# Kernel tuning notes

Hardware: AMD Instinct MI355X
Metric: run time of the kernel (lower is better)

Reference implementation:

```python
import jax, jax.numpy as jnp
import numpy as np

B, N, D, NS, HID, ITERS = 32, 4096, 256, 8, 128, 3
EPS = 1e-8
LN_EPS = 1e-5


def _ln(x, g, b):
    mu = jnp.mean(x, axis=-1, keepdims=True)
    var = jnp.mean(jnp.square(x - mu), axis=-1, keepdims=True)
    return (x - mu) * jax.lax.rsqrt(var + LN_EPS) * g + b


def setup_inputs() -> dict:
    key = jax.random.key(0)
    ks = jax.random.split(key, 32)
    scale = D ** -0.5

    def lin(k, out_d, in_d):
        return jax.random.normal(k, (out_d, in_d), jnp.float32) * (in_d ** -0.5)

    inp = {
        "inputs": jax.random.normal(ks[0], (B, N, D), jnp.float32),
        "slot_noise": jax.random.normal(ks[1], (B, NS, D), jnp.float32),
        "slots_mu": jax.random.uniform(ks[2], (1, 1, D), jnp.float32, -1.0, 1.0) * scale,
        "slots_sigma": jax.random.uniform(ks[3], (1, 1, D), jnp.float32, -1.0, 1.0) * scale,
        "Wq": lin(ks[4], D, D),
        "Wk": lin(ks[5], D, D),
        "Wv": lin(ks[6], D, D),
        "gru_w_ih": lin(ks[7], 3 * D, 2 * D),
        "gru_w_hh": lin(ks[8], 3 * D, D),
        "gru_b_ih": jnp.zeros((3 * D,), jnp.float32),
        "gru_b_hh": jnp.zeros((3 * D,), jnp.float32),
        "obj_w1": lin(ks[9], HID, D),
        "obj_b1": jnp.zeros((HID,), jnp.float32),
        "obj_w2": lin(ks[10], D, HID),
        "obj_b2": jnp.zeros((D,), jnp.float32),
        "rel_w1": lin(ks[11], HID, 2 * D),
        "rel_b1": jnp.zeros((HID,), jnp.float32),
        "rel_w2": lin(ks[12], D, HID),
        "rel_b2": jnp.zeros((D,), jnp.float32),
        "ln_in_g": jnp.ones((D,), jnp.float32),
        "ln_in_b": jnp.zeros((D,), jnp.float32),
        "ln_s_g": jnp.ones((D,), jnp.float32),
        "ln_s_b": jnp.zeros((D,), jnp.float32),
        "ln_ff_g": jnp.ones((D,), jnp.float32),
        "ln_ff_b": jnp.zeros((D,), jnp.float32),
    }
    return inp


def _rel_msg(x, rel_w1, rel_b1, rel_w2, rel_b2):
    # x: (b, n_s, d). rel_mlp(cat(x_i, x_j)) without materializing the concat:
    # split first layer weight into the x_i and x_j halves.
    A = rel_w1[:, :D]   # (hid, d)
    Bm = rel_w1[:, D:]  # (hid, d)
    xa = jnp.einsum('bid,hd->bih', x, A)
    xb = jnp.einsum('bjd,hd->bjh', x, Bm)
    h = jax.nn.relu(xa[:, :, None, :] + xb[:, None, :, :] + rel_b1)  # (b,ns,ns,hid)
    msg = jnp.einsum('bijh,dh->bijd', h, rel_w2) + rel_b2            # (b,ns,ns,d)
    n_s = x.shape[1]
    diag = jnp.eye(n_s, dtype=bool)[None, :, :, None]
    msg = jnp.where(diag, 0.0, msg)
    return msg.sum(axis=2) / (n_s - 1)


def _gru_cell(x, h, w_ih, w_hh, b_ih, b_hh):
    gx = x @ w_ih.T + b_ih  # (B*, 3d)
    gh = h @ w_hh.T + b_hh
    xr, xz, xn = jnp.split(gx, 3, axis=-1)
    hr, hz, hn = jnp.split(gh, 3, axis=-1)
    r = jax.nn.sigmoid(xr + hr)
    z = jax.nn.sigmoid(xz + hz)
    n = jnp.tanh(xn + r * hn)
    return (1.0 - z) * n + z * h


def reference(inputs, slot_noise, slots_mu, slots_sigma, Wq, Wk, Wv,
              gru_w_ih, gru_w_hh, gru_b_ih, gru_b_hh,
              obj_w1, obj_b1, obj_w2, obj_b2,
              rel_w1, rel_b1, rel_w2, rel_b2,
              ln_in_g, ln_in_b, ln_s_g, ln_s_b, ln_ff_g, ln_ff_b):
    b, n, d = inputs.shape
    n_s = slot_noise.shape[1]
    scale = d ** -0.5

    slots = slots_mu + slot_noise * jnp.exp(slots_sigma)  # (b, n_s, d)

    x = _ln(inputs, ln_in_g, ln_in_b)
    k = jnp.einsum('bnd,ed->bne', x, Wk)
    v = jnp.einsum('bnd,ed->bne', x, Wv)

    attns = []
    for _ in range(ITERS):
        slots_prev = slots
        q = jnp.einsum('bid,ed->bie', _ln(slots, ln_s_g, ln_s_b), Wq)
        dots = jnp.einsum('bid,bjd->bij', q, k) * scale        # (b, n_s, n)
        attn = jax.nn.softmax(dots, axis=1) + EPS              # softmax over slots
        attns.append(attn)
        attn_n = attn / attn.sum(axis=-1, keepdims=True)
        updates = jnp.einsum('bjd,bij->bid', v, attn_n)        # (b, n_s, d)
        rel = _rel_msg(slots_prev, rel_w1, rel_b1, rel_w2, rel_b2)
        gin = jnp.concatenate([updates, rel], axis=-1).reshape(b * n_s, 2 * d)
        slots = _gru_cell(gin, slots_prev.reshape(b * n_s, d),
                          gru_w_ih, gru_w_hh, gru_b_ih, gru_b_hh).reshape(b, n_s, d)
        ff = _ln(slots, ln_ff_g, ln_ff_b)
        slots = slots + (jax.nn.relu(ff @ obj_w1.T + obj_b1) @ obj_w2.T + obj_b2)
    return slots, jnp.stack(attns)
```

## Files before the change

kernel.cpp:

```cpp
#include <hip/hip_runtime.h>
#include <hip/hip_bf16.h>
#include <math.h>

static constexpr int Bc   = 32;
static constexpr int Nc   = 4096;
static constexpr int Dc   = 256;
static constexpr int NSc  = 8;
static constexpr int HIDc = 128;
static constexpr int ITERSc = 3;
#define EPSf 1e-8f
#define LN_EPSf 1e-5f

typedef __attribute__((ext_vector_type(8))) short bf16x8;
typedef __attribute__((ext_vector_type(8))) unsigned short u16x8;
typedef __attribute__((ext_vector_type(4))) float f32x4;

__device__ __forceinline__ float bf2f(unsigned int u) {
  return __uint_as_float((u & 0xffffu) << 16);
}

__device__ __forceinline__ unsigned short f2bfu(float f) {
  unsigned int u = __float_as_uint(f);
  unsigned int r = (u + 0x7fffu + ((u >> 16) & 1u)) >> 16;
  return (unsigned short)r;
}

__device__ __forceinline__ void bf8_to_f(uint4 r, float* o) {
  o[0] = bf2f(r.x); o[1] = bf2f(r.x >> 16);
  o[2] = bf2f(r.y); o[3] = bf2f(r.y >> 16);
  o[4] = bf2f(r.z); o[5] = bf2f(r.z >> 16);
  o[6] = bf2f(r.w); o[7] = bf2f(r.w >> 16);
}

__device__ __forceinline__ void gl_lds16(const void* g, void* l) {
  __builtin_amdgcn_global_load_lds(
      (__attribute__((address_space(1))) void*)(g),
      (__attribute__((address_space(3))) void*)(l), 16, 0, 0);
}

__device__ __forceinline__ float block_sum(float v, float* tmp) {
  #pragma unroll
  for (int o = 32; o > 0; o >>= 1) v += __shfl_down(v, o, 64);
  int lane = threadIdx.x & 63, wid = threadIdx.x >> 6;
  __syncthreads();
  if (lane == 0) tmp[wid] = v;
  __syncthreads();
  return tmp[0] + tmp[1] + tmp[2] + tmp[3];
}

__device__ __forceinline__ float sigmf(float x) { return 1.f / (1.f + expf(-x)); }

__global__ __launch_bounds__(256) void k_init_slots(const float* __restrict__ noise,
                                                    const float* __restrict__ mu,
                                                    const float* __restrict__ sigma,
                                                    float* __restrict__ slots) {
  int idx = blockIdx.x * 256 + threadIdx.x;
  int d = idx & (Dc - 1);
  slots[idx] = mu[d] + noise[idx] * expf(sigma[d]);
}

__global__ __launch_bounds__(256) void k_stats(const float* __restrict__ inp,
                                               float2* __restrict__ stats) {
  __shared__ float tmp[4];
  int t = threadIdx.x;
  size_t row0 = (size_t)blockIdx.x * 8;
  for (int r = 0; r < 8; r++) {
    float x = inp[(row0 + r) * Dc + t];
    float s = block_sum(x, tmp);
    float m = s * (1.0f / Dc);
    float dx = x - m;
    float s2 = block_sum(dx * dx, tmp);
    float rs = rsqrtf(s2 * (1.0f / Dc) + LN_EPSf);
    if (t == 0) stats[row0 + r] = make_float2(m, rs);
  }
}

__global__ __launch_bounds__(256) void k_wcvt(const float* __restrict__ Wk,
                                              const float* __restrict__ Wv,
                                              unsigned short* __restrict__ wbuf) {
  int idx = blockIdx.x * 256 + threadIdx.x;
  int n = idx >> 8, k = idx & 255;
  float v = (n < 256) ? Wk[n * 256 + k] : Wv[(n - 256) * 256 + k];
  wbuf[idx] = f2bfu(v);
}

__global__ __launch_bounds__(256) void k_wprep(const float* __restrict__ w_ih,
                                               const float* __restrict__ w_hh,
                                               unsigned short* __restrict__ Wcat) {
  int idx = blockIdx.x * 256 + threadIdx.x;
  int o = idx / 768, c = idx - o * 768;
  float v = (c < 512) ? w_ih[o * 512 + c] : w_hh[o * 256 + (c - 512)];
  Wcat[idx] = f2bfu(v);
}

#define BM 128
#define BN 128
#define BK 64
__global__ __launch_bounds__(256) void k_gemm_kv(const float* __restrict__ inp,
                                                 const float2* __restrict__ stats,
                                                 const float* __restrict__ lng,
                                                 const float* __restrict__ lnb,
                                                 const unsigned short* __restrict__ wbuf,
                                                 unsigned short* __restrict__ kbuf,
                                                 unsigned short* __restrict__ vbuf) {
  __shared__ unsigned short Als[BM * BK];
  __shared__ unsigned short Bls[BN * BK];
  int tid = threadIdx.x;
  int lane = tid & 63, w = tid >> 6;
  int idx16 = lane & 15, quad = lane >> 4;
  int m0 = (blockIdx.x >> 2) * BM;
  int n0 = (blockIdx.x & 3) * BN;
  int wm = w & 1, wn = w >> 1;

  f32x4 acc[4][4];
  #pragma unroll
  for (int i = 0; i < 4; i++)
    #pragma unroll
    for (int j = 0; j < 4; j++) acc[i][j] = (f32x4){0.f, 0.f, 0.f, 0.f};

  for (int kt = 0; kt < 4; kt++) {
    int k0 = kt * BK;
    #pragma unroll
    for (int c = 0; c < 4; c++) {
      int idx = (w * 4 + c) * 64 + lane;
      int row = idx >> 3, lc = idx & 7;
      int gc = lc ^ (row & 7);
      const char* gsrc = (const char*)wbuf + ((size_t)(n0 + row) * 256 + k0) * 2 + gc * 16;
      char* ldst = (char*)Bls + (size_t)(w * 4 + c) * 1024;
      gl_lds16(gsrc, ldst);
    }
    #pragma unroll
    for (int p = 0; p < 4; p++) {
      int idx = p * 256 + tid;
      int row = idx >> 3, c8 = idx & 7;
      const float* src = inp + (size_t)(m0 + row) * 256 + k0 + c8 * 8;
      float2 st = stats[m0 + row];
      float4 x0 = *(const float4*)(src);
      float4 x1 = *(const float4*)(src + 4);
      float4 g0 = *(const float4*)(lng + k0 + c8 * 8);
      float4 g1 = *(const float4*)(lng + k0 + c8 * 8 + 4);
      float4 b0 = *(const float4*)(lnb + k0 + c8 * 8);
      float4 b1 = *(const float4*)(lnb + k0 + c8 * 8 + 4);
      u16x8 pk;
      pk[0] = f2bfu((x0.x - st.x) * st.y * g0.x + b0.x);
      pk[1] = f2bfu((x0.y - st.x) * st.y * g0.y + b0.y);
      pk[2] = f2bfu((x0.z - st.x) * st.y * g0.z + b0.z);
      pk[3] = f2bfu((x0.w - st.x) * st.y * g0.w + b0.w);
      pk[4] = f2bfu((x1.x - st.x) * st.y * g1.x + b1.x);
      pk[5] = f2bfu((x1.y - st.x) * st.y * g1.y + b1.y);
      pk[6] = f2bfu((x1.z - st.x) * st.y * g1.z + b1.z);
      pk[7] = f2bfu((x1.w - st.x) * st.y * g1.w + b1.w);
      int dchunk = c8 ^ (row & 7);
      *(u16x8*)((char*)Als + (size_t)(row * 8 + dchunk) * 16) = pk;
    }
    __syncthreads();
    #pragma unroll
    for (int ks = 0; ks < 2; ks++) {
      bf16x8 af[4], bfr[4];
      int kchunk = ks * 4 + quad;
      #pragma unroll
      for (int mt = 0; mt < 4; mt++) {
        int row = wm * 64 + mt * 16 + idx16;
        af[mt] = *(const bf16x8*)((const char*)Als + (size_t)(row * 8 + (kchunk ^ (row & 7))) * 16);
      }
      #pragma unroll
      for (int nt = 0; nt < 4; nt++) {
        int row = wn * 64 + nt * 16 + idx16;
        bfr[nt] = *(const bf16x8*)((const char*)Bls + (size_t)(row * 8 + (kchunk ^ (row & 7))) * 16);
      }
      #pragma unroll
      for (int mt = 0; mt < 4; mt++)
        #pragma unroll
        for (int nt = 0; nt < 4; nt++)
          acc[mt][nt] = __builtin_amdgcn_mfma_f32_16x16x32_bf16(af[mt], bfr[nt], acc[mt][nt], 0, 0, 0);
    }
    __syncthreads();
  }
  unsigned short* dst = (n0 < 256) ? kbuf : vbuf;
  int coff = (n0 < 256) ? n0 : (n0 - 256);
  #pragma unroll
  for (int mt = 0; mt < 4; mt++) {
    #pragma unroll
    for (int nt = 0; nt < 4; nt++) {
      int gm = m0 + wm * 64 + mt * 16 + quad * 4;
      int col = coff + wn * 64 + nt * 16 + idx16;
      #pragma unroll
      for (int r = 0; r < 4; r++)
        dst[(size_t)(gm + r) * 256 + col] = f2bfu(acc[mt][nt][r]);
    }
  }
}

__global__ __launch_bounds__(256) void k_qproj0(const float* __restrict__ slots,
                                                const float* __restrict__ Wq,
                                                const float* __restrict__ g,
                                                const float* __restrict__ bb_,
                                                float* __restrict__ q,
                                                float* __restrict__ S,
                                                float* __restrict__ updraw) {
  __shared__ float xs[Dc];
  __shared__ float tmp[4];
  int t = threadIdx.x;
  int row = blockIdx.x;
  updraw[row * 256 + t] = 0.f;
  if (blockIdx.x == 0) S[t] = 0.f;
  float x = slots[row * Dc + t];
  float s = block_sum(x, tmp);
  float m = s * (1.0f / Dc);
  float dx = x - m;
  float s2 = block_sum(dx * dx, tmp);
  float rs = rsqrtf(s2 * (1.0f / Dc) + LN_EPSf);
  xs[t] = dx * rs * g[t] + bb_[t];
  __syncthreads();
  float acc = 0.f;
  const float4* wq4 = (const float4*)(Wq + t * Dc);
  for (int d4 = 0; d4 < Dc / 4; d4++) {
    float4 w = wq4[d4];
    float4 x4 = *(const float4*)&xs[d4 * 4];
    acc += w.x * x4.x + w.y * x4.y + w.z * x4.z + w.w * x4.w;
  }
  q[row * Dc + t] = acc;
}

__global__ __launch_bounds__(256) void k_attn(const float* __restrict__ q,
                                              const unsigned short* __restrict__ kbuf,
                                              const unsigned short* __restrict__ vbuf,
                                              float* __restrict__ attn,
                                              float* __restrict__ S,
                                              float* __restrict__ updraw) {
  __shared__ float qs[NSc][Dc];
  __shared__ float at[NSc][512];
  __shared__ float parts[2][NSc][256];
  __shared__ float tmp[4];
  int t = threadIdx.x;
  int b = blockIdx.x >> 3;
  int jc = blockIdx.x & 7;
  for (int x = t; x < NSc * Dc; x += 256) qs[x >> 8][x & 255] = q[b * NSc * Dc + x];
  __syncthreads();
  int jA = jc * 512 + t;
  const unsigned short* k0 = kbuf + ((size_t)b * Nc + jA) * Dc;
  const unsigned short* k1 = k0 + (size_t)256 * Dc;
  float dot[2][NSc];
  #pragma unroll
  for (int jj = 0; jj < 2; jj++)
    #pragma unroll
    for (int i = 0; i < NSc; i++) dot[jj][i] = 0.f;
  for (int d8 = 0; d8 < Dc / 8; d8++) {
    float kv0[8], kv1[8];
    bf8_to_f(*(const uint4*)(k0 + d8 * 8), kv0);
    bf8_to_f(*(const uint4*)(k1 + d8 * 8), kv1);
    #pragma unroll
    for (int i = 0; i < NSc; i++) {
      const float* qr = &qs[i][d8 * 8];
      float s0 = 0.f, s1 = 0.f;
      #pragma unroll
      for (int u = 0; u < 8; u++) { s0 += kv0[u] * qr[u]; s1 += kv1[u] * qr[u]; }
      dot[0][i] += s0; dot[1][i] += s1;
    }
  }
  float a[2][NSc];
  #pragma unroll
  for (int jj = 0; jj < 2; jj++) {
    float m = -1e30f;
    #pragma unroll
    for (int i = 0; i < NSc; i++) { float s = dot[jj][i] * 0.0625f; dot[jj][i] = s; m = fmaxf(m, s); }
    float sum = 0.f;
    #pragma unroll
    for (int i = 0; i < NSc; i++) { float e = expf(dot[jj][i] - m); a[jj][i] = e; sum += e; }
    float inv = 1.f / sum;
    #pragma unroll
    for (int i = 0; i < NSc; i++) a[jj][i] = a[jj][i] * inv + EPSf;
  }
  float* ab = attn + (size_t)b * NSc * Nc;
  #pragma unroll
  for (int i = 0; i < NSc; i++) {
    ab[i * Nc + jA] = a[0][i];
    ab[i * Nc + jA + 256] = a[1][i];
    at[i][t] = a[0][i];
    at[i][t + 256] = a[1][i];
  }
  for (int i = 0; i < NSc; i++) {
    float bs = block_sum(a[0][i] + a[1][i], tmp);
    if (t == 0) atomicAdd(&S[b * NSc + i], bs);
  }
  __syncthreads();
  int rs = t >> 7, dg = t & 127;
  float acc[NSc][2];
  #pragma unroll
  for (int i = 0; i < NSc; i++) { acc[i][0] = 0.f; acc[i][1] = 0.f; }
  const unsigned short* vr = vbuf + ((size_t)b * Nc + jc * 512 + rs * 256) * Dc + dg * 2;
  for (int j = 0; j < 256; j++) {
    unsigned int vv = *(const unsigned int*)(vr + (size_t)j * Dc);
    float v0 = bf2f(vv), v1 = bf2f(vv >> 16);
    #pragma unroll
    for (int i = 0; i < NSc; i++) {
      float a_ = at[i][rs * 256 + j];
      acc[i][0] += a_ * v0;
      acc[i][1] += a_ * v1;
    }
  }
  #pragma unroll
  for (int i = 0; i < NSc; i++) {
    parts[rs][i][dg * 2] = acc[i][0];
    parts[rs][i][dg * 2 + 1] = acc[i][1];
  }
  __syncthreads();
  for (int i = 0; i < NSc; i++) {
    float val = parts[0][i][t] + parts[1][i][t];
    atomicAdd(&updraw[(b * NSc + i) * 256 + t], val);
  }
}

__global__ __launch_bounds__(256) void k_slot_a(const float* __restrict__ slots,
                                                const float* __restrict__ updraw,
                                                const float* __restrict__ S,
                                                const float* __restrict__ w1,
                                                const float* __restrict__ b1,
                                                const float* __restrict__ w2,
                                                const float* __restrict__ b2,
                                                unsigned short* __restrict__ Xb) {
  __shared__ float sp[NSc][256];
  __shared__ float xa[4][128];
  __shared__ float xb[NSc][128];
  __shared__ float hs[4][128];
  int t = threadIdx.x;
  int b = blockIdx.x >> 1, half = blockIdx.x & 1;
  int i0 = half * 4;
  for (int x = t; x < NSc * 256; x += 256) sp[x >> 8][x & 255] = slots[b * NSc * 256 + x];
  __syncthreads();
  for (int r = 0; r < 4; r++) {
    int grow = b * NSc + i0 + r;
    float u = updraw[grow * 256 + t] / S[grow];
    Xb[(size_t)grow * 768 + t] = f2bfu(u);
    Xb[(size_t)grow * 768 + 512 + t] = f2bfu(sp[i0 + r][t]);
  }
  int h = t & 127;
  {
    int jg = t >> 7;
    const float* wr = w1 + h * 512 + 256;
    float acc[4] = {0.f, 0.f, 0.f, 0.f};
    for (int d = 0; d < 256; d += 4) {
      float4 wv = *(const float4*)(wr + d);
      #pragma unroll
      for (int j = 0; j < 4; j++) {
        const float* s4 = &sp[jg * 4 + j][d];
        acc[j] += wv.x * s4[0] + wv.y * s4[1] + wv.z * s4[2] + wv.w * s4[3];
      }
    }
    #pragma unroll
    for (int j = 0; j < 4; j++) xb[jg * 4 + j][h] = acc[j];
  }
  {
    int rg = t >> 7;
    const float* wr = w1 + h * 512;
    float acc[2] = {0.f, 0.f};
    for (int d = 0; d < 256; d += 4) {
      float4 wv = *(const float4*)(wr + d);
      #pragma unroll
      for (int rr = 0; rr < 2; rr++) {
        const float* s4 = &sp[i0 + rg * 2 + rr][d];
        acc[rr] += wv.x * s4[0] + wv.y * s4[1] + wv.z * s4[2] + wv.w * s4[3];
      }
    }
    #pragma unroll
    for (int rr = 0; rr < 2; rr++) xa[rg * 2 + rr][h] = acc[rr];
  }
  __syncthreads();
  {
    float bv = b1[h];
    int ig = t >> 7;
    #pragma unroll
    for (int ii = 0; ii < 2; ii++) {
      int il = ig * 2 + ii;
      int ibatch = i0 + il;
      float av = xa[il][h];
      float s = 0.f;
      #pragma unroll
      for (int j = 0; j < NSc; j++) {
        if (j == ibatch) continue;
        s += fmaxf(av + xb[j][h] + bv, 0.f);
      }
      hs[il][h] = s;
    }
  }
  __syncthreads();
  {
    const float* w2r = w2 + t * 128;
    float acc[4] = {0.f, 0.f, 0.f, 0.f};
    for (int hh = 0; hh < 128; hh += 4) {
      float4 wv = *(const float4*)(w2r + hh);
      #pragma unroll
      for (int r = 0; r < 4; r++) {
        const float* h4 = &hs[r][hh];
        acc[r] += wv.x * h4[0] + wv.y * h4[1] + wv.z * h4[2] + wv.w * h4[3];
      }
    }
    float bv2 = b2[t];
    for (int r = 0; r < 4; r++) {
      float rel = acc[r] * (1.0f / 7.0f) + bv2;
      Xb[(size_t)(b * NSc + i0 + r) * 768 + 256 + t] = f2bfu(rel);
    }
  }
}

__global__ __launch_bounds__(256) void k_gates(const unsigned short* __restrict__ Xb,
                                               const unsigned short* __restrict__ Wcat,
                                               unsigned short* __restrict__ Yb) {
  __shared__ unsigned short Als[64 * 64];
  __shared__ unsigned short Bls[64 * 64];
  int tid = threadIdx.x;
  int lane = tid & 63, w = tid >> 6;
  int idx16 = lane & 15, quad = lane >> 4;
  int m0 = (blockIdx.x / 12) * 64;
  int n0 = (blockIdx.x % 12) * 64;
  int wm = w & 1, wn = w >> 1;
  f32x4 acc[2][2];
  #pragma unroll
  for (int i = 0; i < 2; i++)
    #pragma unroll
    for (int j = 0; j < 2; j++) acc[i][j] = (f32x4){0.f, 0.f, 0.f, 0.f};

  for (int kt = 0; kt < 12; kt++) {
    int k0 = kt * 64;
    #pragma unroll
    for (int c = 0; c < 2; c++) {
      int idx = (w * 2 + c) * 64 + lane;
      int row = idx >> 3, lc = idx & 7;
      int gc = lc ^ (row & 7);
      gl_lds16((const char*)Xb + (size_t)(m0 + row) * 1536 + k0 * 2 + gc * 16,
               (char*)Als + (size_t)(w * 2 + c) * 1024);
      gl_lds16((const char*)Wcat + (size_t)(n0 + row) * 1536 + k0 * 2 + gc * 16,
               (char*)Bls + (size_t)(w * 2 + c) * 1024);
    }
    __syncthreads();
    #pragma unroll
    for (int ks = 0; ks < 2; ks++) {
      bf16x8 af[2], bfr[2];
      int kchunk = ks * 4 + quad;
      #pragma unroll
      for (int mt = 0; mt < 2; mt++) {
        int row = wm * 32 + mt * 16 + idx16;
        af[mt] = *(const bf16x8*)((const char*)Als + (size_t)(row * 8 + (kchunk ^ (row & 7))) * 16);
      }
      #pragma unroll
      for (int nt = 0; nt < 2; nt++) {
        int row = wn * 32 + nt * 16 + idx16;
        bfr[nt] = *(const bf16x8*)((const char*)Bls + (size_t)(row * 8 + (kchunk ^ (row & 7))) * 16);
      }
      #pragma unroll
      for (int mt = 0; mt < 2; mt++)
        #pragma unroll
        for (int nt = 0; nt < 2; nt++)
          acc[mt][nt] = __builtin_amdgcn_mfma_f32_16x16x32_bf16(af[mt], bfr[nt], acc[mt][nt], 0, 0, 0);
    }
    __syncthreads();
  }
  #pragma unroll
  for (int mt = 0; mt < 2; mt++) {
    #pragma unroll
    for (int nt = 0; nt < 2; nt++) {
      int gm = m0 + wm * 32 + mt * 16 + quad * 4;
      int col = n0 + wn * 32 + nt * 16 + idx16;
      #pragma unroll
      for (int r = 0; r < 4; r++)
        Yb[(size_t)(gm + r) * 768 + col] = f2bfu(acc[mt][nt][r]);
    }
  }
}

__global__ __launch_bounds__(256) void k_slot_c(const unsigned short* __restrict__ Yb,
                                                const float* __restrict__ w_hh,
                                                const float* __restrict__ b_ih,
                                                const float* __restrict__ b_hh,
                                                float* __restrict__ slots,
                                                const float* __restrict__ ow1,
                                                const float* __restrict__ ob1,
                                                const float* __restrict__ ow2,
                                                const float* __restrict__ ob2,
                                                const float* __restrict__ lng,
                                                const float* __restrict__ lnb,
                                                const float* __restrict__ lsg,
                                                const float* __restrict__ lsb,
                                                const float* __restrict__ Wq,
                                                float* __restrict__ qbuf,
                                                float* __restrict__ updraw,
                                                float* __restrict__ S,
                                                float* __restrict__ outf,
                                                int wfinal) {
  __shared__ float sp4[4][256];
  __shared__ float ffl[4][256];
  __shared__ float h1l[4][128];
  __shared__ float xs2[4][256];
  __shared__ float tmp[4];
  int t = threadIdx.x;
  int g0 = blockIdx.x * 4;
  for (int x = t; x < 1024; x += 256) sp4[x >> 8][x & 255] = slots[(size_t)g0 * 256 + x];
  __syncthreads();
  float hn_raw[4] = {0.f, 0.f, 0.f, 0.f};
  {
    const float* whr = w_hh + (size_t)(512 + t) * 256;
    for (int d = 0; d < 256; d += 4) {
      float4 wv = *(const float4*)(whr + d);
      #pragma unroll
      for (int r = 0; r < 4; r++) {
        const float* s4 = &sp4[r][d];
        hn_raw[r] += wv.x * s4[0] + wv.y * s4[1] + wv.z * s4[2] + wv.w * s4[3];
      }
    }
  }
  float bir = b_ih[t], bhr = b_hh[t];
  float biz = b_ih[256 + t], bhz = b_hh[256 + t];
  float bin_ = b_ih[512 + t], bhn = b_hh[512 + t];
  float snew[4];
  #pragma unroll
  for (int r = 0; r < 4; r++) {
    size_t yoff = (size_t)(g0 + r) * 768;
    float yr = bf2f((unsigned int)Yb[yoff + t]);
    float yz = bf2f((unsigned int)Yb[yoff + 256 + t]);
    float yx = bf2f((unsigned int)Yb[yoff + 512 + t]);
    float rg = sigmf(yr + bir + bhr);
    float zg = sigmf(yz + biz + bhz);
    float hn = hn_raw[r] + bhn;
    float xn = (yx - hn_raw[r]) + bin_;
    float ng = tanhf(xn + rg * hn);
    snew[r] = (1.f - zg) * ng + zg * sp4[r][t];
  }
  for (int r = 0; r < 4; r++) {
    float s = block_sum(snew[r], tmp);
    float m = s * (1.0f / 256.0f);
    float dx = snew[r] - m;
    float s2 = block_sum(dx * dx, tmp);
    float rs = rsqrtf(s2 * (1.0f / 256.0f) + LN_EPSf);
    ffl[r][t] = dx * rs * lng[t] + lnb[t];
  }
  __syncthreads();
  {
    int h = t & 127, rg2 = t >> 7;
    const float* w1r = ow1 + h * 256;
    float acc[2] = {0.f, 0.f};
    for (int d = 0; d < 256; d += 4) {
      float4 wv = *(const float4*)(w1r + d);
      #pragma unroll
      for (int rr = 0; rr < 2; rr++) {
        const float* f4 = &ffl[rg2 * 2 + rr][d];
        acc[rr] += wv.x * f4[0] + wv.y * f4[1] + wv.z * f4[2] + wv.w * f4[3];
      }
    }
    float bo = ob1[h];
    #pragma unroll
    for (int rr = 0; rr < 2; rr++) h1l[rg2 * 2 + rr][h] = fmaxf(acc[rr] + bo, 0.f);
  }
  __syncthreads();
  float res[4];
  {
    const float* w2r = ow2 + t * 128;
    float acc[4] = {0.f, 0.f, 0.f, 0.f};
    for (int hh = 0; hh < 128; hh += 4) {
      float4 wv = *(const float4*)(w2r + hh);
      #pragma unroll
      for (int r = 0; r < 4; r++) {
        const float* h4 = &h1l[r][hh];
        acc[r] += wv.x * h4[0] + wv.y * h4[1] + wv.z * h4[2] + wv.w * h4[3];
      }
    }
    float bo2 = ob2[t];
    #pragma unroll
    for (int r = 0; r < 4; r++) res[r] = snew[r] + acc[r] + bo2;
  }
  #pragma unroll
  for (int r = 0; r < 4; r++) {
    slots[(size_t)(g0 + r) * 256 + t] = res[r];
    if (wfinal) outf[(size_t)(g0 + r) * 256 + t] = res[r];
  }
  for (int r = 0; r < 4; r++) {
    float s = block_sum(res[r], tmp);
    float m = s * (1.0f / 256.0f);
    float dx = res[r] - m;
    float s2 = block_sum(dx * dx, tmp);
    float rs = rsqrtf(s2 * (1.0f / 256.0f) + LN_EPSf);
    xs2[r][t] = dx * rs * lsg[t] + lsb[t];
  }
  __syncthreads();
  {
    const float* wqr = Wq + t * 256;
    float acc[4] = {0.f, 0.f, 0.f, 0.f};
    for (int d = 0; d < 256; d += 4) {
      float4 wv = *(const float4*)(wqr + d);
      #pragma unroll
      for (int r = 0; r < 4; r++) {
        const float* x4 = &xs2[r][d];
        acc[r] += wv.x * x4[0] + wv.y * x4[1] + wv.z * x4[2] + wv.w * x4[3];
      }
    }
    #pragma unroll
    for (int r = 0; r < 4; r++) qbuf[(size_t)(g0 + r) * 256 + t] = acc[r];
  }
  #pragma unroll
  for (int r = 0; r < 4; r++) updraw[(size_t)(g0 + r) * 256 + t] = 0.f;
  if (t < 4) S[g0 + t] = 0.f;
}

extern "C" void kernel_launch(void* const* d_in, const int* in_sizes, int n_in,
                              void* d_out, int out_size, void* d_ws, size_t ws_size,
                              hipStream_t stream) {
  const float* inputs      = (const float*)d_in[0];
  const float* slot_noise  = (const float*)d_in[1];
  const float* slots_mu    = (const float*)d_in[2];
  const float* slots_sigma = (const float*)d_in[3];
  const float* Wq          = (const float*)d_in[4];
  const float* Wk          = (const float*)d_in[5];
  const float* Wv          = (const float*)d_in[6];
  const float* gru_w_ih    = (const float*)d_in[7];
  const float* gru_w_hh    = (const float*)d_in[8];
  const float* gru_b_ih    = (const float*)d_in[9];
  const float* gru_b_hh    = (const float*)d_in[10];
  const float* obj_w1      = (const float*)d_in[11];
  const float* obj_b1      = (const float*)d_in[12];
  const float* obj_w2      = (const float*)d_in[13];
  const float* obj_b2      = (const float*)d_in[14];
  const float* rel_w1      = (const float*)d_in[15];
  const float* rel_b1      = (const float*)d_in[16];
  const float* rel_w2      = (const float*)d_in[17];
  const float* rel_b2      = (const float*)d_in[18];
  const float* ln_in_g     = (const float*)d_in[19];
  const float* ln_in_b     = (const float*)d_in[20];
  const float* ln_s_g      = (const float*)d_in[21];
  const float* ln_s_b      = (const float*)d_in[22];
  const float* ln_ff_g     = (const float*)d_in[23];
  const float* ln_ff_b     = (const float*)d_in[24];

  char* w = (char*)d_ws;
  unsigned short* kbuf = (unsigned short*)(w);
  unsigned short* vbuf = (unsigned short*)(w + (size_t)67108864);
  float* qbuf   = (float*)(w + (size_t)134217728);
  float* slots  = (float*)(w + (size_t)134479872);
  float* updraw = (float*)(w + (size_t)134742016);
  float* Sbuf   = (float*)(w + (size_t)135004160);
  unsigned short* Wcat = (unsigned short*)(w + (size_t)135008256);
  float2* stats = (float2*)(w + (size_t)135008256);
  unsigned short* Xbuf = (unsigned short*)(w + (size_t)136187904);
  unsigned short* wbuf = (unsigned short*)(w + (size_t)136187904);
  unsigned short* Ybuf = (unsigned short*)(w + (size_t)136581120);

  float* out = (float*)d_out;
  float* attn_base = out + (size_t)Bc * NSc * Dc;

  k_init_slots<<<Bc * NSc * Dc / 256, 256, 0, stream>>>(slot_noise, slots_mu, slots_sigma, slots);
  k_wcvt<<<512, 256, 0, stream>>>(Wk, Wv, wbuf);
  k_stats<<<Bc * Nc / 8, 256, 0, stream>>>(inputs, stats);
  k_gemm_kv<<<(Bc * Nc / BM) * 4, 256, 0, stream>>>(inputs, stats, ln_in_g, ln_in_b,
                                                    wbuf, kbuf, vbuf);
  k_wprep<<<768 * 768 / 256, 256, 0, stream>>>(gru_w_ih, gru_w_hh, Wcat);
  k_qproj0<<<Bc * NSc, 256, 0, stream>>>(slots, Wq, ln_s_g, ln_s_b, qbuf, Sbuf, updraw);

  for (int it = 0; it < ITERSc; it++) {
    float* attn = attn_base + (size_t)it * Bc * NSc * Nc;
    k_attn<<<Bc * 8, 256, 0, stream>>>(qbuf, kbuf, vbuf, attn, Sbuf, updraw);
    k_slot_a<<<Bc * 2, 256, 0, stream>>>(slots, updraw, Sbuf,
                                         rel_w1, rel_b1, rel_w2, rel_b2, Xbuf);
    k_gates<<<4 * 12, 256, 0, stream>>>(Xbuf, Wcat, Ybuf);
    k_slot_c<<<64, 256, 0, stream>>>(Ybuf, gru_w_hh, gru_b_ih, gru_b_hh, slots,
                                     obj_w1, obj_b1, obj_w2, obj_b2,
                                     ln_ff_g, ln_ff_b, ln_s_g, ln_s_b, Wq,
                                     qbuf, updraw, Sbuf,
                                     out, it == ITERSc - 1 ? 1 : 0);
  }
}
```

Baseline: 771.4 us.

## Fuse input LayerNorm stats into KV GEMM, pre-transpose small weights to bf16, retile attention

The separate LayerNorm statistics pass is removed: the KV GEMM now computes per-row mean and rstd itself with wave shuffles and uses 64-row tiles covering all 512 K/V output columns, so the input is read once per tile. Small weights (rel, obj, Wq, the W_hh n-gate block) are pre-transposed and converted to bf16 in a new prep kernel, giving coalesced reads in the slot kernels. The attention kernel now runs twice as many blocks, each handling 256 tokens, and q is stored as bf16. LayerNorms in the slot kernels switch to single-pass shuffle reductions, which trades some numerical accuracy (one-pass variance, bf16 weights and q) for less memory traffic and fewer barriers.

```diff
diff --git a/kernel.cpp b/kernel.cpp
--- a/kernel.cpp
+++ b/kernel.cpp
@@ -15,6 +15,15 @@
 typedef __attribute__((ext_vector_type(8))) unsigned short u16x8;
 typedef __attribute__((ext_vector_type(4))) float f32x4;
 
+static constexpr int W1AT = 0;
+static constexpr int W1BT = 32768;
+static constexpr int W2T  = 65536;
+static constexpr int OW1T = 98304;
+static constexpr int OW2T = 131072;
+static constexpr int WQT  = 163840;
+static constexpr int WHNT = 229376;
+static constexpr int TW_ELEMS = 294912;
+
 __device__ __forceinline__ float bf2f(unsigned int u) {
   return __uint_as_float((u & 0xffffu) << 16);
 }
@@ -59,22 +68,6 @@
   slots[idx] = mu[d] + noise[idx] * expf(sigma[d]);
 }
 
-__global__ __launch_bounds__(256) void k_stats(const float* __restrict__ inp,
-                                               float2* __restrict__ stats) {
-  __shared__ float tmp[4];
-  int t = threadIdx.x;
-  size_t row0 = (size_t)blockIdx.x * 8;
-  for (int r = 0; r < 8; r++) {
-    float x = inp[(row0 + r) * Dc + t];
-    float s = block_sum(x, tmp);
-    float m = s * (1.0f / Dc);
-    float dx = x - m;
-    float s2 = block_sum(dx * dx, tmp);
-    float rs = rsqrtf(s2 * (1.0f / Dc) + LN_EPSf);
-    if (t == 0) stats[row0 + r] = make_float2(m, rs);
-  }
-}
-
 __global__ __launch_bounds__(256) void k_wcvt(const float* __restrict__ Wk,
                                               const float* __restrict__ Wv,
                                               unsigned short* __restrict__ wbuf) {
@@ -89,52 +82,85 @@
                                                unsigned short* __restrict__ Wcat) {
   int idx = blockIdx.x * 256 + threadIdx.x;
   int o = idx / 768, c = idx - o * 768;
-  float v = (c < 512) ? w_ih[o * 512 + c] : w_hh[o * 256 + (c - 512)];
+  float v;
+  if (c < 512) v = w_ih[o * 512 + c];
+  else v = (o < 512) ? w_hh[o * 256 + (c - 512)] : 0.f;
   Wcat[idx] = f2bfu(v);
 }
 
-#define BM 128
-#define BN 128
-#define BK 64
-__global__ __launch_bounds__(256) void k_gemm_kv(const float* __restrict__ inp,
-                                                 const float2* __restrict__ stats,
-                                                 const float* __restrict__ lng,
-                                                 const float* __restrict__ lnb,
-                                                 const unsigned short* __restrict__ wbuf,
-                                                 unsigned short* __restrict__ kbuf,
-                                                 unsigned short* __restrict__ vbuf) {
-  __shared__ unsigned short Als[BM * BK];
-  __shared__ unsigned short Bls[BN * BK];
+__global__ __launch_bounds__(256) void k_tprep(const float* __restrict__ rel_w1,
+                                               const float* __restrict__ rel_w2,
+                                               const float* __restrict__ obj_w1,
+                                               const float* __restrict__ obj_w2,
+                                               const float* __restrict__ Wq,
+                                               const float* __restrict__ w_hh,
+                                               unsigned short* __restrict__ Tw) {
+  int i = blockIdx.x * 256 + threadIdx.x;
+  if (i >= TW_ELEMS) return;
+  float v;
+  if (i < W1BT) { int j = i - W1AT; int d = j >> 7, h = j & 127; v = rel_w1[h * 512 + d]; }
+  else if (i < W2T)  { int j = i - W1BT; int d = j >> 7, h = j & 127; v = rel_w1[h * 512 + 256 + d]; }
+  else if (i < OW1T) { int j = i - W2T;  int h = j >> 8, o = j & 255; v = rel_w2[o * 128 + h]; }
+  else if (i < OW2T) { int j = i - OW1T; int d = j >> 7, h = j & 127; v = obj_w1[h * 256 + d]; }
+  else if (i < WQT)  { int j = i - OW2T; int h = j >> 8, o = j & 255; v = obj_w2[o * 128 + h]; }
+  else if (i < WHNT) { int j = i - WQT;  int d = j >> 8, e = j & 255; v = Wq[e * 256 + d]; }
+  else               { int j = i - WHNT; int d = j >> 8, o = j & 255; v = w_hh[(512 + o) * 256 + d]; }
+  Tw[i] = f2bfu(v);
+}
+
+__global__ __launch_bounds__(256, 2) void k_gemm_kv(const float* __restrict__ inp,
+                                                    const float* __restrict__ lng,
+                                                    const float* __restrict__ lnb,
+                                                    const unsigned short* __restrict__ wbuf,
+                                                    unsigned short* __restrict__ kbuf,
+                                                    unsigned short* __restrict__ vbuf) {
+  __shared__ unsigned short Als[64 * 64];
+  __shared__ unsigned short Bls[512 * 64];
+  __shared__ float smu[64];
+  __shared__ float srs[64];
   int tid = threadIdx.x;
   int lane = tid & 63, w = tid >> 6;
   int idx16 = lane & 15, quad = lane >> 4;
-  int m0 = (blockIdx.x >> 2) * BM;
-  int n0 = (blockIdx.x & 3) * BN;
-  int wm = w & 1, wn = w >> 1;
-
-  f32x4 acc[4][4];
+  int m0 = blockIdx.x * 64;
+
+  for (int rr = 0; rr < 16; rr++) {
+    int row = w * 16 + rr;
+    float4 v = *(const float4*)(inp + (size_t)(m0 + row) * 256 + lane * 4);
+    float s = v.x + v.y + v.z + v.w;
+    float q = v.x * v.x + v.y * v.y + v.z * v.z + v.w * v.w;
+    #pragma unroll
+    for (int o = 32; o > 0; o >>= 1) { s += __shfl_down(s, o, 64); q += __shfl_down(q, o, 64); }
+    if (lane == 0) {
+      float mu = s * (1.0f / 256.0f);
+      float var = q * (1.0f / 256.0f) - mu * mu;
+      smu[row] = mu;
+      srs[row] = rsqrtf(var + LN_EPSf);
+    }
+  }
+  __syncthreads();
+
+  f32x4 acc[4][8];
   #pragma unroll
   for (int i = 0; i < 4; i++)
     #pragma unroll
-    for (int j = 0; j < 4; j++) acc[i][j] = (f32x4){0.f, 0.f, 0.f, 0.f};
+    for (int j = 0; j < 8; j++) acc[i][j] = (f32x4){0.f, 0.f, 0.f, 0.f};
 
   for (int kt = 0; kt < 4; kt++) {
-    int k0 = kt * BK;
-    #pragma unroll
-    for (int c = 0; c < 4; c++) {
-      int idx = (w * 4 + c) * 64 + lane;
+    int k0 = kt * 64;
+    #pragma unroll
+    for (int c = 0; c < 16; c++) {
+      int idx = (w * 16 + c) * 64 + lane;
       int row = idx >> 3, lc = idx & 7;
       int gc = lc ^ (row & 7);
-      const char* gsrc = (const char*)wbuf + ((size_t)(n0 + row) * 256 + k0) * 2 + gc * 16;
-      char* ldst = (char*)Bls + (size_t)(w * 4 + c) * 1024;
-      gl_lds16(gsrc, ldst);
-    }
-    #pragma unroll
-    for (int p = 0; p < 4; p++) {
+      gl_lds16((const char*)wbuf + ((size_t)row * 256 + k0) * 2 + gc * 16,
+               (char*)Bls + (size_t)(w * 16 + c) * 1024);
+    }
+    #pragma unroll
+    for (int p = 0; p < 2; p++) {
       int idx = p * 256 + tid;
       int row = idx >> 3, c8 = idx & 7;
       const float* src = inp + (size_t)(m0 + row) * 256 + k0 + c8 * 8;
-      float2 st = stats[m0 + row];
+      float mu = smu[row], rs = srs[row];
       float4 x0 = *(const float4*)(src);
       float4 x1 = *(const float4*)(src + 4);
       float4 g0 = *(const float4*)(lng + k0 + c8 * 8);
@@ -142,60 +168,60 @@
       float4 b0 = *(const float4*)(lnb + k0 + c8 * 8);
       float4 b1 = *(const float4*)(lnb + k0 + c8 * 8 + 4);
       u16x8 pk;
-      pk[0] = f2bfu((x0.x - st.x) * st.y * g0.x + b0.x);
-      pk[1] = f2bfu((x0.y - st.x) * st.y * g0.y + b0.y);
-      pk[2] = f2bfu((x0.z - st.x) * st.y * g0.z + b0.z);
-      pk[3] = f2bfu((x0.w - st.x) * st.y * g0.w + b0.w);
-      pk[4] = f2bfu((x1.x - st.x) * st.y * g1.x + b1.x);
-      pk[5] = f2bfu((x1.y - st.x) * st.y * g1.y + b1.y);
-      pk[6] = f2bfu((x1.z - st.x) * st.y * g1.z + b1.z);
-      pk[7] = f2bfu((x1.w - st.x) * st.y * g1.w + b1.w);
+      pk[0] = f2bfu((x0.x - mu) * rs * g0.x + b0.x);
+      pk[1] = f2bfu((x0.y - mu) * rs * g0.y + b0.y);
+      pk[2] = f2bfu((x0.z - mu) * rs * g0.z + b0.z);
+      pk[3] = f2bfu((x0.w - mu) * rs * g0.w + b0.w);
+      pk[4] = f2bfu((x1.x - mu) * rs * g1.x + b1.x);
+      pk[5] = f2bfu((x1.y - mu) * rs * g1.y + b1.y);
+      pk[6] = f2bfu((x1.z - mu) * rs * g1.z + b1.z);
+      pk[7] = f2bfu((x1.w - mu) * rs * g1.w + b1.w);
       int dchunk = c8 ^ (row & 7);
       *(u16x8*)((char*)Als + (size_t)(row * 8 + dchunk) * 16) = pk;
     }
     __syncthreads();
     #pragma unroll
     for (int ks = 0; ks < 2; ks++) {
-      bf16x8 af[4], bfr[4];
       int kchunk = ks * 4 + quad;
+      bf16x8 af[4], bfr[8];
       #pragma unroll
       for (int mt = 0; mt < 4; mt++) {
-        int row = wm * 64 + mt * 16 + idx16;
+        int row = mt * 16 + idx16;
         af[mt] = *(const bf16x8*)((const char*)Als + (size_t)(row * 8 + (kchunk ^ (row & 7))) * 16);
       }
       #pragma unroll
-      for (int nt = 0; nt < 4; nt++) {
-        int row = wn * 64 + nt * 16 + idx16;
+      for (int nt = 0; nt < 8; nt++) {
+        int row = w * 128 + nt * 16 + idx16;
         bfr[nt] = *(const bf16x8*)((const char*)Bls + (size_t)(row * 8 + (kchunk ^ (row & 7))) * 16);
       }
       #pragma unroll
       for (int mt = 0; mt < 4; mt++)
         #pragma unroll
-        for (int nt = 0; nt < 4; nt++)
+        for (int nt = 0; nt < 8; nt++)
           acc[mt][nt] = __builtin_amdgcn_mfma_f32_16x16x32_bf16(af[mt], bfr[nt], acc[mt][nt], 0, 0, 0);
     }
     __syncthreads();
   }
-  unsigned short* dst = (n0 < 256) ? kbuf : vbuf;
-  int coff = (n0 < 256) ? n0 : (n0 - 256);
   #pragma unroll
   for (int mt = 0; mt < 4; mt++) {
     #pragma unroll
-    for (int nt = 0; nt < 4; nt++) {
-      int gm = m0 + wm * 64 + mt * 16 + quad * 4;
-      int col = coff + wn * 64 + nt * 16 + idx16;
+    for (int nt = 0; nt < 8; nt++) {
+      int gm = m0 + mt * 16 + quad * 4;
+      int col = w * 128 + nt * 16 + idx16;
+      unsigned short* dst = (col < 256) ? kbuf : vbuf;
+      int c = col & 255;
       #pragma unroll
       for (int r = 0; r < 4; r++)
-        dst[(size_t)(gm + r) * 256 + col] = f2bfu(acc[mt][nt][r]);
+        dst[(size_t)(gm + r) * 256 + c] = f2bfu(acc[mt][nt][r]);
     }
   }
 }
 
 __global__ __launch_bounds__(256) void k_qproj0(const float* __restrict__ slots,
-                                                const float* __restrict__ Wq,
+                                                const unsigned short* __restrict__ Tw,
                                                 const float* __restrict__ g,
                                                 const float* __restrict__ bb_,
-                                                float* __restrict__ q,
+                                                unsigned short* __restrict__ qb,
                                                 float* __restrict__ S,
                                                 float* __restrict__ updraw) {
   __shared__ float xs[Dc];
@@ -213,96 +239,93 @@
   xs[t] = dx * rs * g[t] + bb_[t];
   __syncthreads();
   float acc = 0.f;
-  const float4* wq4 = (const float4*)(Wq + t * Dc);
-  for (int d4 = 0; d4 < Dc / 4; d4++) {
-    float4 w = wq4[d4];
-    float4 x4 = *(const float4*)&xs[d4 * 4];
-    acc += w.x * x4.x + w.y * x4.y + w.z * x4.z + w.w * x4.w;
-  }
-  q[row * Dc + t] = acc;
-}
-
-__global__ __launch_bounds__(256) void k_attn(const float* __restrict__ q,
+  const unsigned short* wq = Tw + WQT;
+  for (int d = 0; d < 256; d++) acc += bf2f(wq[d * 256 + t]) * xs[d];
+  qb[row * 256 + t] = f2bfu(acc);
+}
+
+__global__ __launch_bounds__(256) void k_attn(const unsigned short* __restrict__ qb,
                                               const unsigned short* __restrict__ kbuf,
                                               const unsigned short* __restrict__ vbuf,
                                               float* __restrict__ attn,
                                               float* __restrict__ S,
                                               float* __restrict__ updraw) {
   __shared__ float qs[NSc][Dc];
-  __shared__ float at[NSc][512];
+  __shared__ float at[NSc][256];
   __shared__ float parts[2][NSc][256];
-  __shared__ float tmp[4];
   int t = threadIdx.x;
-  int b = blockIdx.x >> 3;
-  int jc = blockIdx.x & 7;
-  for (int x = t; x < NSc * Dc; x += 256) qs[x >> 8][x & 255] = q[b * NSc * Dc + x];
-  __syncthreads();
-  int jA = jc * 512 + t;
-  const unsigned short* k0 = kbuf + ((size_t)b * Nc + jA) * Dc;
-  const unsigned short* k1 = k0 + (size_t)256 * Dc;
-  float dot[2][NSc];
-  #pragma unroll
-  for (int jj = 0; jj < 2; jj++)
-    #pragma unroll
-    for (int i = 0; i < NSc; i++) dot[jj][i] = 0.f;
+  int b = blockIdx.x >> 4;
+  int jc = blockIdx.x & 15;
+  int j0 = jc * 256;
+  for (int x = t; x < NSc * Dc; x += 256) qs[x >> 8][x & 255] = bf2f(qb[b * NSc * Dc + x]);
+  __syncthreads();
+  int j = j0 + t;
+  const uint4* krow = (const uint4*)(kbuf + ((size_t)b * Nc + j) * Dc);
+  float dot[NSc];
+  #pragma unroll
+  for (int i = 0; i < NSc; i++) dot[i] = 0.f;
   for (int d8 = 0; d8 < Dc / 8; d8++) {
-    float kv0[8], kv1[8];
-    bf8_to_f(*(const uint4*)(k0 + d8 * 8), kv0);
-    bf8_to_f(*(const uint4*)(k1 + d8 * 8), kv1);
+    float kv[8];
+    bf8_to_f(krow[d8], kv);
     #pragma unroll
     for (int i = 0; i < NSc; i++) {
       const float* qr = &qs[i][d8 * 8];
-      float s0 = 0.f, s1 = 0.f;
-      #pragma unroll
-      for (int u = 0; u < 8; u++) { s0 += kv0[u] * qr[u]; s1 += kv1[u] * qr[u]; }
-      dot[0][i] += s0; dot[1][i] += s1;
-    }
-  }
-  float a[2][NSc];
-  #pragma unroll
-  for (int jj = 0; jj < 2; jj++) {
-    float m = -1e30f;
-    #pragma unroll
-    for (int i = 0; i < NSc; i++) { float s = dot[jj][i] * 0.0625f; dot[jj][i] = s; m = fmaxf(m, s); }
-    float sum = 0.f;
-    #pragma unroll
-    for (int i = 0; i < NSc; i++) { float e = expf(dot[jj][i] - m); a[jj][i] = e; sum += e; }
-    float inv = 1.f / sum;
-    #pragma unroll
-    for (int i = 0; i < NSc; i++) a[jj][i] = a[jj][i] * inv + EPSf;
-  }
+      float s0 = 0.f;
+      #pragma unroll
+      for (int u = 0; u < 8; u++) s0 += kv[u] * qr[u];
+      dot[i] += s0;
+    }
+  }
+  float m = -1e30f;
+  #pragma unroll
+  for (int i = 0; i < NSc; i++) { float s = dot[i] * 0.0625f; dot[i] = s; m = fmaxf(m, s); }
+  float sum = 0.f;
+  float a[NSc];
+  #pragma unroll
+  for (int i = 0; i < NSc; i++) { float e = expf(dot[i] - m); a[i] = e; sum += e; }
+  float inv = 1.f / sum;
+  #pragma unroll
+  for (int i = 0; i < NSc; i++) a[i] = a[i] * inv + EPSf;
   float* ab = attn + (size_t)b * NSc * Nc;
   #pragma unroll
   for (int i = 0; i < NSc; i++) {
-    ab[i * Nc + jA] = a[0][i];
-    ab[i * Nc + jA + 256] = a[1][i];
-    at[i][t] = a[0][i];
-    at[i][t + 256] = a[1][i];
-  }
+    ab[i * Nc + j] = a[i];
+    at[i][t] = a[i];
+  }
+  __syncthreads();
+  {
+    int wv = t >> 6, lane = t & 63;
+    #pragma unroll
+    for (int ii = 0; ii < 2; ii++) {
+      int i = wv + ii * 4;
+      float4 v = *(const float4*)&at[i][lane * 4];
+      float s = v.x + v.y + v.z + v.w;
+      #pragma unroll
+      for (int o = 32; o > 0; o >>= 1) s += __shfl_down(s, o, 64);
+      if (lane == 0) atomicAdd(&S[b * NSc + i], s);
+    }
+  }
+  int rsh = t >> 7, dg = t & 127;
+  float acc[NSc][2];
+  #pragma unroll
+  for (int i = 0; i < NSc; i++) { acc[i][0] = 0.f; acc[i][1] = 0.f; }
+  const unsigned short* vr = vbuf + ((size_t)b * Nc + j0 + rsh * 128) * Dc + dg * 2;
+  for (int jj = 0; jj < 128; jj += 2) {
+    unsigned int v0 = *(const unsigned int*)(vr + (size_t)jj * Dc);
+    unsigned int v1 = *(const unsigned int*)(vr + (size_t)(jj + 1) * Dc);
+    float v0a = bf2f(v0), v0b = bf2f(v0 >> 16);
+    float v1a = bf2f(v1), v1b = bf2f(v1 >> 16);
+    #pragma unroll
+    for (int i = 0; i < NSc; i++) {
+      float2 ap = *(const float2*)&at[i][rsh * 128 + jj];
+      acc[i][0] += ap.x * v0a + ap.y * v1a;
+      acc[i][1] += ap.x * v0b + ap.y * v1b;
+    }
+  }
+  #pragma unroll
   for (int i = 0; i < NSc; i++) {
-    float bs = block_sum(a[0][i] + a[1][i], tmp);
-    if (t == 0) atomicAdd(&S[b * NSc + i], bs);
-  }
-  __syncthreads();
-  int rs = t >> 7, dg = t & 127;
-  float acc[NSc][2];
-  #pragma unroll
-  for (int i = 0; i < NSc; i++) { acc[i][0] = 0.f; acc[i][1] = 0.f; }
-  const unsigned short* vr = vbuf + ((size_t)b * Nc + jc * 512 + rs * 256) * Dc + dg * 2;
-  for (int j = 0; j < 256; j++) {
-    unsigned int vv = *(const unsigned int*)(vr + (size_t)j * Dc);
-    float v0 = bf2f(vv), v1 = bf2f(vv >> 16);
-    #pragma unroll
-    for (int i = 0; i < NSc; i++) {
-      float a_ = at[i][rs * 256 + j];
-      acc[i][0] += a_ * v0;
-      acc[i][1] += a_ * v1;
-    }
-  }
-  #pragma unroll
-  for (int i = 0; i < NSc; i++) {
-    parts[rs][i][dg * 2] = acc[i][0];
-    parts[rs][i][dg * 2 + 1] = acc[i][1];
+    parts[rsh][i][dg * 2] = acc[i][0];
+    parts[rsh][i][dg * 2 + 1] = acc[i][1];
   }
   __syncthreads();
   for (int i = 0; i < NSc; i++) {
@@ -314,14 +337,13 @@
 __global__ __launch_bounds__(256) void k_slot_a(const float* __restrict__ slots,
                                                 const float* __restrict__ updraw,
                                                 const float* __restrict__ S,
-                                                const float* __restrict__ w1,
+                                                const unsigned short* __restrict__ Tw,
                                                 const float* __restrict__ b1,
-                                                const float* __restrict__ w2,
                                                 const float* __restrict__ b2,
                                                 unsigned short* __restrict__ Xb) {
   __shared__ float sp[NSc][256];
-  __shared__ float xa[4][128];
-  __shared__ float xb[NSc][128];
+  __shared__ float xpart[2][12][128];
+  __shared__ float xabl[12][128];
   __shared__ float hs[4][128];
   int t = threadIdx.x;
   int b = blockIdx.x >> 1, half = blockIdx.x & 1;
@@ -334,36 +356,31 @@
     Xb[(size_t)grow * 768 + t] = f2bfu(u);
     Xb[(size_t)grow * 768 + 512 + t] = f2bfu(sp[i0 + r][t]);
   }
-  int h = t & 127;
-  {
-    int jg = t >> 7;
-    const float* wr = w1 + h * 512 + 256;
-    float acc[4] = {0.f, 0.f, 0.f, 0.f};
-    for (int d = 0; d < 256; d += 4) {
-      float4 wv = *(const float4*)(wr + d);
-      #pragma unroll
-      for (int j = 0; j < 4; j++) {
-        const float* s4 = &sp[jg * 4 + j][d];
-        acc[j] += wv.x * s4[0] + wv.y * s4[1] + wv.z * s4[2] + wv.w * s4[3];
-      }
-    }
-    #pragma unroll
-    for (int j = 0; j < 4; j++) xb[jg * 4 + j][h] = acc[j];
-  }
-  {
-    int rg = t >> 7;
-    const float* wr = w1 + h * 512;
-    float acc[2] = {0.f, 0.f};
-    for (int d = 0; d < 256; d += 4) {
-      float4 wv = *(const float4*)(wr + d);
-      #pragma unroll
-      for (int rr = 0; rr < 2; rr++) {
-        const float* s4 = &sp[i0 + rg * 2 + rr][d];
-        acc[rr] += wv.x * s4[0] + wv.y * s4[1] + wv.z * s4[2] + wv.w * s4[3];
-      }
-    }
-    #pragma unroll
-    for (int rr = 0; rr < 2; rr++) xa[rg * 2 + rr][h] = acc[rr];
+  int h = t & 127, dh = t >> 7;
+  {
+    const unsigned short* wa = Tw + W1AT;
+    const unsigned short* wb = Tw + W1BT;
+    float accb[8] = {0, 0, 0, 0, 0, 0, 0, 0};
+    float acca[4] = {0, 0, 0, 0};
+    for (int dd = 0; dd < 128; dd++) {
+      int d = dh * 128 + dd;
+      float wbv = bf2f(wb[d * 128 + h]);
+      float wav = bf2f(wa[d * 128 + h]);
+      #pragma unroll
+      for (int jj = 0; jj < 8; jj++) accb[jj] += wbv * sp[jj][d];
+      #pragma unroll
+      for (int r = 0; r < 4; r++) acca[r] += wav * sp[i0 + r][d];
+    }
+    #pragma unroll
+    for (int jj = 0; jj < 8; jj++) xpart[dh][jj][h] = accb[jj];
+    #pragma unroll
+    for (int r = 0; r < 4; r++) xpart[dh][8 + r][h] = acca[r];
+  }
+  __syncthreads();
+  {
+    int g = t >> 7;
+    for (int jj = g * 6; jj < g * 6 + 6; jj++)
+      xabl[jj][h] = xpart[0][jj][h] + xpart[1][jj][h];
   }
   __syncthreads();
   {
@@ -373,31 +390,28 @@
     for (int ii = 0; ii < 2; ii++) {
       int il = ig * 2 + ii;
       int ibatch = i0 + il;
-      float av = xa[il][h];
+      float av = xabl[8 + il][h];
       float s = 0.f;
       #pragma unroll
-      for (int j = 0; j < NSc; j++) {
-        if (j == ibatch) continue;
-        s += fmaxf(av + xb[j][h] + bv, 0.f);
+      for (int jj = 0; jj < NSc; jj++) {
+        if (jj == ibatch) continue;
+        s += fmaxf(av + xabl[jj][h] + bv, 0.f);
       }
       hs[il][h] = s;
     }
   }
   __syncthreads();
   {
-    const float* w2r = w2 + t * 128;
-    float acc[4] = {0.f, 0.f, 0.f, 0.f};
-    for (int hh = 0; hh < 128; hh += 4) {
-      float4 wv = *(const float4*)(w2r + hh);
-      #pragma unroll
-      for (int r = 0; r < 4; r++) {
-        const float* h4 = &hs[r][hh];
-        acc[r] += wv.x * h4[0] + wv.y * h4[1] + wv.z * h4[2] + wv.w * h4[3];
-      }
+    const unsigned short* w2 = Tw + W2T;
+    float am[4] = {0, 0, 0, 0};
+    for (int hh = 0; hh < 128; hh++) {
+      float wv = bf2f(w2[hh * 256 + t]);
+      #pragma unroll
+      for (int r = 0; r < 4; r++) am[r] += wv * hs[r][hh];
     }
     float bv2 = b2[t];
     for (int r = 0; r < 4; r++) {
-      float rel = acc[r] * (1.0f / 7.0f) + bv2;
+      float rel = am[r] * (1.0f / 7.0f) + bv2;
       Xb[(size_t)(b * NSc + i0 + r) * 768 + 256 + t] = f2bfu(rel);
     }
   }
@@ -469,43 +483,37 @@
 }
 
 __global__ __launch_bounds__(256) void k_slot_c(const unsigned short* __restrict__ Yb,
-                                                const float* __restrict__ w_hh,
+                                                const unsigned short* __restrict__ Tw,
                                                 const float* __restrict__ b_ih,
                                                 const float* __restrict__ b_hh,
                                                 float* __restrict__ slots,
-                                                const float* __restrict__ ow1,
                                                 const float* __restrict__ ob1,
-                                                const float* __restrict__ ow2,
                                                 const float* __restrict__ ob2,
                                                 const float* __restrict__ lng,
                                                 const float* __restrict__ lnb,
                                                 const float* __restrict__ lsg,
                                                 const float* __restrict__ lsb,
-                                                const float* __restrict__ Wq,
-                                                float* __restrict__ qbuf,
+                                                unsigned short* __restrict__ qb,
                                                 float* __restrict__ updraw,
                                                 float* __restrict__ S,
                                                 float* __restrict__ outf,
                                                 int wfinal) {
   __shared__ float sp4[4][256];
   __shared__ float ffl[4][256];
+  __shared__ float h1p[2][4][128];
   __shared__ float h1l[4][128];
   __shared__ float xs2[4][256];
-  __shared__ float tmp[4];
   int t = threadIdx.x;
   int g0 = blockIdx.x * 4;
   for (int x = t; x < 1024; x += 256) sp4[x >> 8][x & 255] = slots[(size_t)g0 * 256 + x];
   __syncthreads();
-  float hn_raw[4] = {0.f, 0.f, 0.f, 0.f};
-  {
-    const float* whr = w_hh + (size_t)(512 + t) * 256;
-    for (int d = 0; d < 256; d += 4) {
-      float4 wv = *(const float4*)(whr + d);
-      #pragma unroll
-      for (int r = 0; r < 4; r++) {
-        const float* s4 = &sp4[r][d];
-        hn_raw[r] += wv.x * s4[0] + wv.y * s4[1] + wv.z * s4[2] + wv.w * s4[3];
-      }
+  float hn[4] = {0, 0, 0, 0};
+  {
+    const unsigned short* wh = Tw + WHNT;
+    for (int d = 0; d < 256; d++) {
+      float wv = bf2f(wh[d * 256 + t]);
+      #pragma unroll
+      for (int r = 0; r < 4; r++) hn[r] += wv * sp4[r][d];
     }
   }
   float bir = b_ih[t], bhr = b_hh[t];
@@ -520,80 +528,105 @@
     float yx = bf2f((unsigned int)Yb[yoff + 512 + t]);
     float rg = sigmf(yr + bir + bhr);
     float zg = sigmf(yz + biz + bhz);
-    float hn = hn_raw[r] + bhn;
-    float xn = (yx - hn_raw[r]) + bin_;
-    float ng = tanhf(xn + rg * hn);
+    float ng = tanhf(yx + bin_ + rg * (hn[r] + bhn));
     snew[r] = (1.f - zg) * ng + zg * sp4[r][t];
-  }
-  for (int r = 0; r < 4; r++) {
-    float s = block_sum(snew[r], tmp);
-    float m = s * (1.0f / 256.0f);
-    float dx = snew[r] - m;
-    float s2 = block_sum(dx * dx, tmp);
-    float rs = rsqrtf(s2 * (1.0f / 256.0f) + LN_EPSf);
-    ffl[r][t] = dx * rs * lng[t] + lnb[t];
-  }
-  __syncthreads();
-  {
-    int h = t & 127, rg2 = t >> 7;
-    const float* w1r = ow1 + h * 256;
-    float acc[2] = {0.f, 0.f};
-    for (int d = 0; d < 256; d += 4) {
-      float4 wv = *(const float4*)(w1r + d);
-      #pragma unroll
-      for (int rr = 0; rr < 2; rr++) {
-        const float* f4 = &ffl[rg2 * 2 + rr][d];
-        acc[rr] += wv.x * f4[0] + wv.y * f4[1] + wv.z * f4[2] + wv.w * f4[3];
-      }
-    }
+    ffl[r][t] = snew[r];
+  }
+  __syncthreads();
+  {
+    int wv = t >> 6, lane = t & 63;
+    float4 v = *(const float4*)&ffl[wv][lane * 4];
+    float s = v.x + v.y + v.z + v.w;
+    float q = v.x * v.x + v.y * v.y + v.z * v.z + v.w * v.w;
+    #pragma unroll
+    for (int o = 32; o > 0; o >>= 1) { s += __shfl_down(s, o, 64); q += __shfl_down(q, o, 64); }
+    s = __shfl(s, 0, 64); q = __shfl(q, 0, 64);
+    float mu = s * (1.0f / 256.0f);
+    float rs = rsqrtf(q * (1.0f / 256.0f) - mu * mu + LN_EPSf);
+    float4 g4 = *(const float4*)&lng[lane * 4];
+    float4 b4 = *(const float4*)&lnb[lane * 4];
+    float4 o4;
+    o4.x = (v.x - mu) * rs * g4.x + b4.x;
+    o4.y = (v.y - mu) * rs * g4.y + b4.y;
+    o4.z = (v.z - mu) * rs * g4.z + b4.z;
+    o4.w = (v.w - mu) * rs * g4.w + b4.w;
+    *(float4*)&ffl[wv][lane * 4] = o4;
+  }
+  __syncthreads();
+  {
+    const unsigned short* w1 = Tw + OW1T;
+    int h = t & 127, dh = t >> 7;
+    float a1[4] = {0, 0, 0, 0};
+    for (int dd = 0; dd < 128; dd++) {
+      int d = dh * 128 + dd;
+      float wv = bf2f(w1[d * 128 + h]);
+      #pragma unroll
+      for (int r = 0; r < 4; r++) a1[r] += wv * ffl[r][d];
+    }
+    #pragma unroll
+    for (int r = 0; r < 4; r++) h1p[dh][r][h] = a1[r];
+  }
+  __syncthreads();
+  {
+    int h = t & 127, g = t >> 7;
     float bo = ob1[h];
     #pragma unroll
-    for (int rr = 0; rr < 2; rr++) h1l[rg2 * 2 + rr][h] = fmaxf(acc[rr] + bo, 0.f);
+    for (int rr = 0; rr < 2; rr++) {
+      int r = g * 2 + rr;
+      h1l[r][h] = fmaxf(h1p[0][r][h] + h1p[1][r][h] + bo, 0.f);
+    }
   }
   __syncthreads();
   float res[4];
   {
-    const float* w2r = ow2 + t * 128;
-    float acc[4] = {0.f, 0.f, 0.f, 0.f};
-    for (int hh = 0; hh < 128; hh += 4) {
-      float4 wv = *(const float4*)(w2r + hh);
-      #pragma unroll
-      for (int r = 0; r < 4; r++) {
-        const float* h4 = &h1l[r][hh];
-        acc[r] += wv.x * h4[0] + wv.y * h4[1] + wv.z * h4[2] + wv.w * h4[3];
-      }
+    const unsigned short* w2 = Tw + OW2T;
+    float ao[4] = {0, 0, 0, 0};
+    for (int hh = 0; hh < 128; hh++) {
+      float wv = bf2f(w2[hh * 256 + t]);
+      #pragma unroll
+      for (int r = 0; r < 4; r++) ao[r] += wv * h1l[r][hh];
     }
     float bo2 = ob2[t];
     #pragma unroll
-    for (int r = 0; r < 4; r++) res[r] = snew[r] + acc[r] + bo2;
+    for (int r = 0; r < 4; r++) res[r] = snew[r] + ao[r] + bo2;
   }
   #pragma unroll
   for (int r = 0; r < 4; r++) {
     slots[(size_t)(g0 + r) * 256 + t] = res[r];
     if (wfinal) outf[(size_t)(g0 + r) * 256 + t] = res[r];
-  }
-  for (int r = 0; r < 4; r++) {
-    float s = block_sum(res[r], tmp);
-    float m = s * (1.0f / 256.0f);
-    float dx = res[r] - m;
-    float s2 = block_sum(dx * dx, tmp);
-    float rs = rsqrtf(s2 * (1.0f / 256.0f) + LN_EPSf);
-    xs2[r][t] = dx * rs * lsg[t] + lsb[t];
-  }
-  __syncthreads();
-  {
-    const float* wqr = Wq + t * 256;
-    float acc[4] = {0.f, 0.f, 0.f, 0.f};
-    for (int d = 0; d < 256; d += 4) {
-      float4 wv = *(const float4*)(wqr + d);
-      #pragma unroll
-      for (int r = 0; r < 4; r++) {
-        const float* x4 = &xs2[r][d];
-        acc[r] += wv.x * x4[0] + wv.y * x4[1] + wv.z * x4[2] + wv.w * x4[3];
-      }
-    }
-    #pragma unroll
-    for (int r = 0; r < 4; r++) qbuf[(size_t)(g0 + r) * 256 + t] = acc[r];
+    xs2[r][t] = res[r];
+  }
+  __syncthreads();
+  {
+    int wv = t >> 6, lane = t & 63;
+    float4 v = *(const float4*)&xs2[wv][lane * 4];
+    float s = v.x + v.y + v.z + v.w;
+    float q = v.x * v.x + v.y * v.y + v.z * v.z + v.w * v.w;
+    #pragma unroll
+    for (int o = 32; o > 0; o >>= 1) { s += __shfl_down(s, o, 64); q += __shfl_down(q, o, 64); }
+    s = __shfl(s, 0, 64); q = __shfl(q, 0, 64);
+    float mu = s * (1.0f / 256.0f);
+    float rs = rsqrtf(q * (1.0f / 256.0f) - mu * mu + LN_EPSf);
+    float4 g4 = *(const float4*)&lsg[lane * 4];
+    float4 b4 = *(const float4*)&lsb[lane * 4];
+    float4 o4;
+    o4.x = (v.x - mu) * rs * g4.x + b4.x;
+    o4.y = (v.y - mu) * rs * g4.y + b4.y;
+    o4.z = (v.z - mu) * rs * g4.z + b4.z;
+    o4.w = (v.w - mu) * rs * g4.w + b4.w;
+    *(float4*)&xs2[wv][lane * 4] = o4;
+  }
+  __syncthreads();
+  {
+    const unsigned short* wq = Tw + WQT;
+    float aq[4] = {0, 0, 0, 0};
+    for (int d = 0; d < 256; d++) {
+      float wv = bf2f(wq[d * 256 + t]);
+      #pragma unroll
+      for (int r = 0; r < 4; r++) aq[r] += wv * xs2[r][d];
+    }
+    #pragma unroll
+    for (int r = 0; r < 4; r++) qb[(size_t)(g0 + r) * 256 + t] = f2bfu(aq[r]);
   }
   #pragma unroll
   for (int r = 0; r < 4; r++) updraw[(size_t)(g0 + r) * 256 + t] = 0.f;
@@ -632,37 +665,34 @@
   char* w = (char*)d_ws;
   unsigned short* kbuf = (unsigned short*)(w);
   unsigned short* vbuf = (unsigned short*)(w + (size_t)67108864);
-  float* qbuf   = (float*)(w + (size_t)134217728);
-  float* slots  = (float*)(w + (size_t)134479872);
-  float* updraw = (float*)(w + (size_t)134742016);
-  float* Sbuf   = (float*)(w + (size_t)135004160);
-  unsigned short* Wcat = (unsigned short*)(w + (size_t)135008256);
-  float2* stats = (float2*)(w + (size_t)135008256);
-  unsigned short* Xbuf = (unsigned short*)(w + (size_t)136187904);
-  unsigned short* wbuf = (unsigned short*)(w + (size_t)136187904);
-  unsigned short* Ybuf = (unsigned short*)(w + (size_t)136581120);
+  float* slots  = (float*)(w + (size_t)134217728);
+  float* updraw = (float*)(w + (size_t)134479872);
+  float* Sbuf   = (float*)(w + (size_t)134742016);
+  unsigned short* Wcat = (unsigned short*)(w + (size_t)134743040);
+  unsigned short* Tw   = (unsigned short*)(w + (size_t)135922688);
+  unsigned short* Xbuf = (unsigned short*)(w + (size_t)136512512);
+  unsigned short* qb   = (unsigned short*)(w + (size_t)136512512);
+  unsigned short* Ybuf = (unsigned short*)(w + (size_t)136905728);
+  unsigned short* wbuf = (unsigned short*)(w + (size_t)136905728);
 
   float* out = (float*)d_out;
   float* attn_base = out + (size_t)Bc * NSc * Dc;
 
   k_init_slots<<<Bc * NSc * Dc / 256, 256, 0, stream>>>(slot_noise, slots_mu, slots_sigma, slots);
   k_wcvt<<<512, 256, 0, stream>>>(Wk, Wv, wbuf);
-  k_stats<<<Bc * Nc / 8, 256, 0, stream>>>(inputs, stats);
-  k_gemm_kv<<<(Bc * Nc / BM) * 4, 256, 0, stream>>>(inputs, stats, ln_in_g, ln_in_b,
-                                                    wbuf, kbuf, vbuf);
   k_wprep<<<768 * 768 / 256, 256, 0, stream>>>(gru_w_ih, gru_w_hh, Wcat);
-  k_qproj0<<<Bc * NSc, 256, 0, stream>>>(slots, Wq, ln_s_g, ln_s_b, qbuf, Sbuf, updraw);
+  k_tprep<<<(TW_ELEMS + 255) / 256, 256, 0, stream>>>(rel_w1, rel_w2, obj_w1, obj_w2, Wq, gru_w_hh, Tw);
+  k_gemm_kv<<<Bc * Nc / 64, 256, 0, stream>>>(inputs, ln_in_g, ln_in_b, wbuf, kbuf, vbuf);
+  k_qproj0<<<Bc * NSc, 256, 0, stream>>>(slots, Tw, ln_s_g, ln_s_b, qb, Sbuf, updraw);
 
   for (int it = 0; it < ITERSc; it++) {
     float* attn = attn_base + (size_t)it * Bc * NSc * Nc;
-    k_attn<<<Bc * 8, 256, 0, stream>>>(qbuf, kbuf, vbuf, attn, Sbuf, updraw);
-    k_slot_a<<<Bc * 2, 256, 0, stream>>>(slots, updraw, Sbuf,
-                                         rel_w1, rel_b1, rel_w2, rel_b2, Xbuf);
+    k_attn<<<Bc * 16, 256, 0, stream>>>(qb, kbuf, vbuf, attn, Sbuf, updraw);
+    k_slot_a<<<Bc * 2, 256, 0, stream>>>(slots, updraw, Sbuf, Tw, rel_b1, rel_b2, Xbuf);
     k_gates<<<4 * 12, 256, 0, stream>>>(Xbuf, Wcat, Ybuf);
-    k_slot_c<<<64, 256, 0, stream>>>(Ybuf, gru_w_hh, gru_b_ih, gru_b_hh, slots,
-                                     obj_w1, obj_b1, obj_w2, obj_b2,
-                                     ln_ff_g, ln_ff_b, ln_s_g, ln_s_b, Wq,
-                                     qbuf, updraw, Sbuf,
+    k_slot_c<<<64, 256, 0, stream>>>(Ybuf, Tw, gru_b_ih, gru_b_hh, slots,
+                                     obj_b1, obj_b2, ln_ff_g, ln_ff_b, ln_s_g, ln_s_b,
+                                     qb, updraw, Sbuf,
                                      out, it == ITERSc - 1 ? 1 : 0);
   }
 }
```

Result: faster. 692.5 us (-10.2%).
